# Performance work log

Measured on AMD Instinct MI355X. Metric: run time of the kernel, lower is better.

Reference implementation:

```python
import jax, jax.numpy as jnp
import numpy as np

B, N, DIN, DOUT, EIN, EOUT = 8, 256, 64, 64, 64, 64


def setup_inputs() -> dict:
    key = jax.random.key(0)
    ks = jax.random.split(key, 9)
    A = jax.random.randint(ks[0], (B, N, N), 0, 2).astype(jnp.float32)  # {0,1} connectivity
    emb_node = jax.random.normal(ks[1], (B, N, DIN), dtype=jnp.float32)
    emb_edge = jax.random.normal(ks[2], (B, N, N, EIN), dtype=jnp.float32)
    s_n = 1.0 / np.sqrt(DIN)
    s_e = 1.0 / np.sqrt(EIN)
    Wn = jax.random.uniform(ks[3], (DIN, DOUT), minval=-s_n, maxval=s_n)
    bn = jax.random.uniform(ks[4], (DOUT,), minval=-s_n, maxval=s_n)
    Wsn = jax.random.uniform(ks[5], (DIN, DOUT), minval=-s_n, maxval=s_n)
    bsn = jax.random.uniform(ks[6], (DOUT,), minval=-s_n, maxval=s_n)
    We = jax.random.uniform(ks[7], (EIN, EOUT), minval=-s_e, maxval=s_e)
    be = jax.random.uniform(ks[8], (EOUT,), minval=-s_e, maxval=s_e)
    return {"A": A, "emb_node": emb_node, "emb_edge": emb_edge,
            "Wn": Wn, "bn": bn, "Wsn": Wsn, "bsn": bsn, "We": We, "be": be}


def reference(A, emb_node, emb_edge, Wn, bn, Wsn, bsn, We, be):
    # mode=1 (default) of ChannelIndependentConv
    node_x = emb_node @ Wn + bn          # [B,N,DOUT]
    node_sx = emb_node @ Wsn + bsn       # [B,N,DOUT]
    edge_x = emb_edge @ We + be          # [B,N,N,EOUT]
    # mask edges by connectivity, then channel-independent aggregation:
    # out[b,i,c] = sum_j A[b,i,j] * edge_x[b,i,j,c] * node_x[b,j,c]
    Ae = A[..., None] * edge_x           # [B,N,N,EOUT]
    agg = jnp.einsum('bijc,bjc->bic', Ae, node_x)  # [B,N,DOUT]
    node_out = jax.nn.relu(agg) + jax.nn.relu(node_sx)
    edge_out = jax.nn.relu(edge_x)
    return node_out, edge_out
```

## Files before the change

kernel.cpp:

```cpp
#include <hip/hip_runtime.h>
#include <hip/hip_bf16.h>

#define BN   2048
#define NN   256
#define CH   64
#define RPC  32
#define NCHK 8
#define LDST 88

typedef __attribute__((ext_vector_type(8))) short short8;
typedef __attribute__((ext_vector_type(4))) short short4v;
typedef __attribute__((ext_vector_type(4))) float fv4;

static __device__ inline short f2bf(float f) {
  unsigned u = __float_as_uint(f);
  u += 0x7FFF + ((u >> 16) & 1);
  return (short)(u >> 16);
}
static __device__ inline short4v cvt4(fv4 v) {
  short4v r;
  r[0] = f2bf(v[0]); r[1] = f2bf(v[1]); r[2] = f2bf(v[2]); r[3] = f2bf(v[3]);
  return r;
}

__global__ __launch_bounds__(256) void node_kernel(
    const float* __restrict__ emb_node, const float* __restrict__ Wn,
    const float* __restrict__ bn, const float* __restrict__ Wsn,
    const float* __restrict__ bsn, float* __restrict__ node_x,
    float* __restrict__ rsx) {
  __shared__ float s_emb[4][CH];
  __shared__ float s_Wn[CH * CH];
  __shared__ float s_Ws[CH * CH];
  const int tid = threadIdx.x;
  const int r = tid >> 6;
  const int c = tid & 63;
  const int row = blockIdx.x * 4 + r;
#pragma unroll
  for (int i = 0; i < 4; ++i) {
    *(fv4*)&s_Wn[(i * 256 + tid) * 4] = *(const fv4*)&Wn[(i * 256 + tid) * 4];
    *(fv4*)&s_Ws[(i * 256 + tid) * 4] = *(const fv4*)&Wsn[(i * 256 + tid) * 4];
  }
  s_emb[r][c] = emb_node[row * CH + c];
  __syncthreads();
  float a1 = bn[c], a2 = bsn[c];
#pragma unroll
  for (int k = 0; k < CH; ++k) {
    const float e = s_emb[r][k];
    a1 = fmaf(e, s_Wn[k * CH + c], a1);
    a2 = fmaf(e, s_Ws[k * CH + c], a2);
  }
  node_x[row * CH + c] = a1;
  rsx[row * CH + c] = fmaxf(a2, 0.0f);
}

__global__ __launch_bounds__(256) void edge_mfma_kernel(
    const float* __restrict__ A, const float* __restrict__ emb_edge,
    const float* __restrict__ We, const float* __restrict__ be,
    const float* __restrict__ node_x, const float* __restrict__ rsx,
    float* __restrict__ node_out, float* __restrict__ edge_out) {
  const int bi   = blockIdx.x;
  const int b    = bi >> 8;
  const int tid  = threadIdx.x;
  const int lane = tid & 63;
  const int wave = tid >> 6;
  const int l15  = lane & 15;
  const int quad = lane >> 4;
  const int c    = wave * 16 + l15;

  __shared__ __align__(16) short sbuf[2][RPC * LDST];
  __shared__ float s_A[NN];

  short8 bfrag[2];
#pragma unroll
  for (int h = 0; h < 2; ++h)
#pragma unroll
    for (int j = 0; j < 8; ++j)
      bfrag[h][j] = f2bf(We[(h * 32 + quad * 8 + j) * CH + c]);
  const float bias = be[c];

  const float* __restrict__ ee = emb_edge + (size_t)bi * NN * CH;
  float*       __restrict__ eo = edge_out + (size_t)bi * NN * CH;
  const float* __restrict__ nx = node_x + (size_t)b * NN * CH;

  s_A[tid] = A[(size_t)bi * NN + tid];

  const int srow = tid >> 4;
  const int kcol = (tid & 15) * 4;

  fv4 st0 = *(const fv4*)(ee + tid * 4);
  fv4 st1 = *(const fv4*)(ee + 1024 + tid * 4);
  *(short4v*)&sbuf[0][srow * LDST + kcol] = cvt4(st0);
  *(short4v*)&sbuf[0][(16 + srow) * LDST + kcol] = cvt4(st1);

  float agg = 0.0f;

#pragma unroll 2
  for (int ch = 0; ch < NCHK; ++ch) {
    const int pb = ch & 1;
    if (ch + 1 < NCHK) {
      const float* cb = ee + (ch + 1) * (RPC * CH);
      st0 = *(const fv4*)(cb + tid * 4);
      st1 = *(const fv4*)(cb + 1024 + tid * 4);
    }
    __syncthreads();

#pragma unroll
    for (int half = 0; half < 2; ++half) {
      const int j0l = half * 16;
      const int j0  = ch * RPC + j0l;
      const fv4 av = *(const fv4*)&s_A[j0 + quad * 4];
      float nxv[4];
#pragma unroll
      for (int r = 0; r < 4; ++r)
        nxv[r] = nx[(j0 + quad * 4 + r) * CH + c];
      const short8 af0 =
          *(const short8*)&sbuf[pb][(j0l + l15) * LDST + quad * 8];
      const short8 af1 =
          *(const short8*)&sbuf[pb][(j0l + l15) * LDST + 32 + quad * 8];
      fv4 acc = {0.0f, 0.0f, 0.0f, 0.0f};
      acc = __builtin_amdgcn_mfma_f32_16x16x32_bf16(af0, bfrag[0], acc, 0, 0, 0);
      acc = __builtin_amdgcn_mfma_f32_16x16x32_bf16(af1, bfrag[1], acc, 0, 0, 0);
#pragma unroll
      for (int r = 0; r < 4; ++r) {
        const int row = j0 + quad * 4 + r;
        const float ex = acc[r] + bias;
        eo[row * CH + c] = fmaxf(ex, 0.0f);
        agg = fmaf(av[r] * ex, nxv[r], agg);
      }
    }

    if (ch + 1 < NCHK) {
      *(short4v*)&sbuf[pb ^ 1][srow * LDST + kcol] = cvt4(st0);
      *(short4v*)&sbuf[pb ^ 1][(16 + srow) * LDST + kcol] = cvt4(st1);
    }
  }

  agg += __shfl_xor(agg, 16, 64);
  agg += __shfl_xor(agg, 32, 64);
  if (quad == 0) {
    node_out[(size_t)bi * CH + c] =
        fmaxf(agg, 0.0f) + rsx[(size_t)bi * CH + c];
  }
}

extern "C" void kernel_launch(void* const* d_in, const int* in_sizes, int n_in,
                              void* d_out, int out_size, void* d_ws, size_t ws_size,
                              hipStream_t stream) {
  const float* A        = (const float*)d_in[0];
  const float* emb_node = (const float*)d_in[1];
  const float* emb_edge = (const float*)d_in[2];
  const float* Wn       = (const float*)d_in[3];
  const float* bn       = (const float*)d_in[4];
  const float* Wsn      = (const float*)d_in[5];
  const float* bsn      = (const float*)d_in[6];
  const float* We       = (const float*)d_in[7];
  const float* be       = (const float*)d_in[8];

  float* node_out = (float*)d_out;
  float* edge_out = (float*)d_out + (size_t)BN * CH;

  float* node_x = (float*)d_ws;
  float* rsx    = (float*)d_ws + (size_t)BN * CH;

  hipLaunchKernelGGL(node_kernel, dim3(BN / 4), dim3(256), 0, stream,
                     emb_node, Wn, bn, Wsn, bsn, node_x, rsx);
  hipLaunchKernelGGL(edge_mfma_kernel, dim3(BN), dim3(256), 0, stream,
                     A, emb_edge, We, be, node_x, rsx, node_out, edge_out);
}
```

Before: 258.0 us.

## Load edge MFMA fragments directly from global, drop LDS staging

Drops the shared-memory double buffer in the edge kernel. Each lane now loads its A-fragment rows straight from global memory and converts them with packed v_cvt_pk_bf16_f32 instructions, so the __syncthreads barriers and LDS traffic go away. The change also folds the bias into the accumulator init, writes edge_out with nontemporal stores, and asks for 8 blocks per CU in the launch bounds. The cost is that the per-lane global loads are less coalesced (strided 32-byte pieces across rows), and the loads are no longer prefetched ahead by a software pipeline.

```diff
diff --git a/kernel.cpp b/kernel.cpp
--- a/kernel.cpp
+++ b/kernel.cpp
@@ -1,15 +1,10 @@
 #include <hip/hip_runtime.h>
-#include <hip/hip_bf16.h>
 
 #define BN   2048
 #define NN   256
 #define CH   64
-#define RPC  32
-#define NCHK 8
-#define LDST 88
 
 typedef __attribute__((ext_vector_type(8))) short short8;
-typedef __attribute__((ext_vector_type(4))) short short4v;
 typedef __attribute__((ext_vector_type(4))) float fv4;
 
 static __device__ inline short f2bf(float f) {
@@ -17,10 +12,14 @@
   u += 0x7FFF + ((u >> 16) & 1);
   return (short)(u >> 16);
 }
-static __device__ inline short4v cvt4(fv4 v) {
-  short4v r;
-  r[0] = f2bf(v[0]); r[1] = f2bf(v[1]); r[2] = f2bf(v[2]); r[3] = f2bf(v[3]);
-  return r;
+
+static __device__ inline short8 cvt_frag(fv4 a, fv4 b) {
+  union { short8 s; unsigned u[4]; } r;
+  asm("v_cvt_pk_bf16_f32 %0, %1, %2" : "=v"(r.u[0]) : "v"(a[0]), "v"(a[1]));
+  asm("v_cvt_pk_bf16_f32 %0, %1, %2" : "=v"(r.u[1]) : "v"(a[2]), "v"(a[3]));
+  asm("v_cvt_pk_bf16_f32 %0, %1, %2" : "=v"(r.u[2]) : "v"(b[0]), "v"(b[1]));
+  asm("v_cvt_pk_bf16_f32 %0, %1, %2" : "=v"(r.u[3]) : "v"(b[2]), "v"(b[3]));
+  return r.s;
 }
 
 __global__ __launch_bounds__(256) void node_kernel(
@@ -53,7 +52,7 @@
   rsx[row * CH + c] = fmaxf(a2, 0.0f);
 }
 
-__global__ __launch_bounds__(256) void edge_mfma_kernel(
+__global__ __launch_bounds__(256, 8) void edge_mfma_kernel(
     const float* __restrict__ A, const float* __restrict__ emb_edge,
     const float* __restrict__ We, const float* __restrict__ be,
     const float* __restrict__ node_x, const float* __restrict__ rsx,
@@ -67,8 +66,10 @@
   const int quad = lane >> 4;
   const int c    = wave * 16 + l15;
 
-  __shared__ __align__(16) short sbuf[2][RPC * LDST];
-  __shared__ float s_A[NN];
+  const float* __restrict__ ee = emb_edge + (size_t)bi * NN * CH;
+  float*       __restrict__ eo = edge_out + (size_t)bi * NN * CH;
+  const float* __restrict__ nx = node_x + (size_t)b * NN * CH;
+  const float* __restrict__ Ar = A + (size_t)bi * NN;
 
   short8 bfrag[2];
 #pragma unroll
@@ -78,60 +79,31 @@
       bfrag[h][j] = f2bf(We[(h * 32 + quad * 8 + j) * CH + c]);
   const float bias = be[c];
 
-  const float* __restrict__ ee = emb_edge + (size_t)bi * NN * CH;
-  float*       __restrict__ eo = edge_out + (size_t)bi * NN * CH;
-  const float* __restrict__ nx = node_x + (size_t)b * NN * CH;
-
-  s_A[tid] = A[(size_t)bi * NN + tid];
-
-  const int srow = tid >> 4;
-  const int kcol = (tid & 15) * 4;
-
-  fv4 st0 = *(const fv4*)(ee + tid * 4);
-  fv4 st1 = *(const fv4*)(ee + 1024 + tid * 4);
-  *(short4v*)&sbuf[0][srow * LDST + kcol] = cvt4(st0);
-  *(short4v*)&sbuf[0][(16 + srow) * LDST + kcol] = cvt4(st1);
-
   float agg = 0.0f;
 
-#pragma unroll 2
-  for (int ch = 0; ch < NCHK; ++ch) {
-    const int pb = ch & 1;
-    if (ch + 1 < NCHK) {
-      const float* cb = ee + (ch + 1) * (RPC * CH);
-      st0 = *(const fv4*)(cb + tid * 4);
-      st1 = *(const fv4*)(cb + 1024 + tid * 4);
-    }
-    __syncthreads();
+  for (int t = 0; t < 16; ++t) {
+    const int j0 = t * 16;
+    const float* rp = ee + (j0 + l15) * CH + quad * 8;
+    const fv4 a0 = *(const fv4*)(rp);
+    const fv4 a1 = *(const fv4*)(rp + 4);
+    const fv4 a2 = *(const fv4*)(rp + 32);
+    const fv4 a3 = *(const fv4*)(rp + 36);
+    const fv4 av = *(const fv4*)(Ar + j0 + quad * 4);
+    const int rb = j0 + quad * 4;
+    float nxv[4];
+#pragma unroll
+    for (int r = 0; r < 4; ++r) nxv[r] = nx[(rb + r) * CH + c];
 
+    const short8 af0 = cvt_frag(a0, a1);
+    const short8 af1 = cvt_frag(a2, a3);
+    fv4 acc = {bias, bias, bias, bias};
+    acc = __builtin_amdgcn_mfma_f32_16x16x32_bf16(af0, bfrag[0], acc, 0, 0, 0);
+    acc = __builtin_amdgcn_mfma_f32_16x16x32_bf16(af1, bfrag[1], acc, 0, 0, 0);
 #pragma unroll
-    for (int half = 0; half < 2; ++half) {
-      const int j0l = half * 16;
-      const int j0  = ch * RPC + j0l;
-      const fv4 av = *(const fv4*)&s_A[j0 + quad * 4];
-      float nxv[4];
-#pragma unroll
-      for (int r = 0; r < 4; ++r)
-        nxv[r] = nx[(j0 + quad * 4 + r) * CH + c];
-      const short8 af0 =
-          *(const short8*)&sbuf[pb][(j0l + l15) * LDST + quad * 8];
-      const short8 af1 =
-          *(const short8*)&sbuf[pb][(j0l + l15) * LDST + 32 + quad * 8];
-      fv4 acc = {0.0f, 0.0f, 0.0f, 0.0f};
-      acc = __builtin_amdgcn_mfma_f32_16x16x32_bf16(af0, bfrag[0], acc, 0, 0, 0);
-      acc = __builtin_amdgcn_mfma_f32_16x16x32_bf16(af1, bfrag[1], acc, 0, 0, 0);
-#pragma unroll
-      for (int r = 0; r < 4; ++r) {
-        const int row = j0 + quad * 4 + r;
-        const float ex = acc[r] + bias;
-        eo[row * CH + c] = fmaxf(ex, 0.0f);
-        agg = fmaf(av[r] * ex, nxv[r], agg);
-      }
-    }
-
-    if (ch + 1 < NCHK) {
-      *(short4v*)&sbuf[pb ^ 1][srow * LDST + kcol] = cvt4(st0);
-      *(short4v*)&sbuf[pb ^ 1][(16 + srow) * LDST + kcol] = cvt4(st1);
+    for (int r = 0; r < 4; ++r) {
+      const float ex = acc[r];
+      __builtin_nontemporal_store(fmaxf(ex, 0.0f), eo + (rb + r) * CH + c);
+      agg = fmaf(av[r] * ex, nxv[r], agg);
     }
   }
 
```

Result: slower. 291.3 us (+12.9%).
